# Kernel tuning notes

Hardware: AMD Instinct MI355X
Metric: run time of the kernel (lower is better)

Reference implementation:

```python
import jax, jax.numpy as jnp
import numpy as np

NB, HD, NL, NF = 5, 64, 4, 10           # num_bins, hidden_dim(d_model), num_layers, num_frames
DI, DS, DC, DTR = 128, 16, 4, 4          # d_inner=2*HD, d_state, d_conv, dt_rank=ceil(HD/16)
B, H, W = 4, 64, 64


def _conv2d(x, w, b):
    y = jax.lax.conv_general_dilated(x, w, (1, 1), 'SAME',
                                     dimension_numbers=('NCHW', 'OIHW', 'NCHW'))
    return y + b[None, :, None, None]


def _bn_relu(x, gamma, beta, eps=1e-5):
    # BatchNorm2d in training mode: biased batch stats over (N,H,W)
    mean = x.mean(axis=(0, 2, 3), keepdims=True)
    var = x.var(axis=(0, 2, 3), keepdims=True)
    y = (x - mean) * jax.lax.rsqrt(var + eps)
    return jax.nn.relu(y * gamma[None, :, None, None] + beta[None, :, None, None])


def _silu(x):
    return x * jax.nn.sigmoid(x)


def _causal_dwconv(x, w, b):
    # x: (B,L,DI), w: (DI,K) depthwise causal conv, b: (DI,)
    K = w.shape[1]
    L = x.shape[1]
    xp = jnp.pad(x, ((0, 0), (K - 1, 0), (0, 0)))
    y = sum(xp[:, k:k + L, :] * w[:, k] for k in range(K))
    return y + b


def _selective_scan(u, delta, A, Bm, Cm, D):
    # u,delta: (B,L,DI); A: (DI,DS); Bm,Cm: (B,L,DS); D: (DI,)
    dT, BT, CT, uT = (t.transpose(1, 0, 2) for t in (delta, Bm, Cm, u))
    h0 = jnp.zeros((u.shape[0], A.shape[0], A.shape[1]), u.dtype)

    def step(h, inp):
        d_t, B_t, C_t, u_t = inp                     # (B,DI),(B,DS),(B,DS),(B,DI)
        dA = jnp.exp(d_t[:, :, None] * A)            # (B,DI,DS)
        h = dA * h + (d_t * u_t)[:, :, None] * B_t[:, None, :]
        y = jnp.einsum('bds,bs->bd', h, C_t)
        return h, y

    _, ys = jax.lax.scan(step, h0, (dT, BT, CT, uT))  # ys: (L,B,DI)
    return ys.transpose(1, 0, 2) + u * D


def _mamba(x, in_proj, conv_w, conv_b, x_proj, dt_w, dt_b, A_log, Dp, out_proj):
    xz = x @ in_proj.T                               # (B,L,2*DI)
    xi, z = jnp.split(xz, 2, axis=-1)
    xi = _silu(_causal_dwconv(xi, conv_w, conv_b))
    xdbc = xi @ x_proj.T                             # (B,L,DTR+2*DS)
    dt, Bm, Cm = jnp.split(xdbc, [DTR, DTR + DS], axis=-1)
    delta = jax.nn.softplus(dt @ dt_w.T + dt_b)
    A = -jnp.exp(A_log)
    y = _selective_scan(xi, delta, A, Bm, Cm, Dp)
    return (y * _silu(z)) @ out_proj.T


def setup_inputs() -> dict:
    key = jax.random.key(0)
    ks = jax.random.split(key, 20)
    s = 0.02
    inp = {
        'x': jax.random.normal(ks[0], (B, NB, H, W), jnp.float32),
        'enc_w': jax.random.normal(ks[1], (HD, NB, 3, 3), jnp.float32) * s,
        'enc_b': jnp.zeros((HD,), jnp.float32),
        'enc_g': jnp.ones((HD,), jnp.float32),
        'enc_be': jnp.zeros((HD,), jnp.float32),
        'in_proj': jax.random.normal(ks[2], (NL, 2 * DI, HD), jnp.float32) * s,
        'conv_w': jax.random.normal(ks[3], (NL, DI, DC), jnp.float32) * s,
        'conv_b': jnp.zeros((NL, DI), jnp.float32),
        'x_proj': jax.random.normal(ks[4], (NL, DTR + 2 * DS, DI), jnp.float32) * s,
        'dt_w': jax.random.normal(ks[5], (NL, DI, DTR), jnp.float32) * s,
        'dt_b': jax.random.normal(ks[6], (NL, DI), jnp.float32) * 0.1 - 4.0,
        'A_log': jnp.broadcast_to(jnp.log(jnp.arange(1, DS + 1, dtype=jnp.float32)),
                                  (NL, DI, DS)).copy(),
        'Dp': jnp.ones((NL, DI), jnp.float32),
        'out_proj': jax.random.normal(ks[7], (NL, HD, DI), jnp.float32) * s,
        'dec1_w': jax.random.normal(ks[8], (HD, HD, 3, 3), jnp.float32) * s,
        'dec1_b': jnp.zeros((HD,), jnp.float32),
        'dec1_g': jnp.ones((HD,), jnp.float32),
        'dec1_be': jnp.zeros((HD,), jnp.float32),
        'dec2_w': jax.random.normal(ks[9], (NF, HD, 3, 3), jnp.float32) * s,
        'dec2_b': jnp.zeros((NF,), jnp.float32),
    }
    return inp


def reference(x, enc_w, enc_b, enc_g, enc_be, in_proj, conv_w, conv_b, x_proj,
              dt_w, dt_b, A_log, Dp, out_proj, dec1_w, dec1_b, dec1_g, dec1_be,
              dec2_w, dec2_b):
    Bb, _, Hh, Ww = x.shape
    h = _bn_relu(_conv2d(x, enc_w, enc_b), enc_g, enc_be)   # (B,HD,H,W)
    t = h.reshape(Bb, HD, Hh * Ww).transpose(0, 2, 1)        # (B,L,HD)
    for i in range(NL):
        t = t + _mamba(t, in_proj[i], conv_w[i], conv_b[i], x_proj[i],
                       dt_w[i], dt_b[i], A_log[i], Dp[i], out_proj[i])
    h = t.transpose(0, 2, 1).reshape(Bb, HD, Hh, Ww)
    h = _bn_relu(_conv2d(h, dec1_w, dec1_b), dec1_g, dec1_be)
    return _conv2d(h, dec2_w, dec2_b)                        # (B,NF,H,W)
```

## Files before the change

kernel.cpp:

```cpp
#include <hip/hip_runtime.h>
#include <hip/hip_bf16.h>

#define BB   4
#define NBC  5
#define HD   64
#define NLAYER 4
#define NFC  10
#define DIM  128
#define DSN  16
#define DCN  4
#define DTRK 4
#define HH   64
#define WWD  64
#define LL   4096
#define MM   (BB*LL)
#define NCHUNK 128
#define CLEN   32
#define TSTEP  16

__global__ void k_prep_all(const float* __restrict__ in_proj, const float* __restrict__ out_proj,
                           const float* __restrict__ dec1_w, const float* __restrict__ dec2_w,
                           float* __restrict__ wTin, float* __restrict__ wTout,
                           float* __restrict__ wT1, float* __restrict__ wT2,
                           float* __restrict__ stats, float* __restrict__ stats2) {
    int idx = blockIdx.x * blockDim.x + threadIdx.x;
    if (idx < 65536) {
        int n = idx & 255, k = (idx >> 8) & 63, l = idx >> 14;
        wTin[idx] = in_proj[(l << 14) + (n << 6) + k];
    } else if (idx < 98304) {
        int j = idx - 65536;
        int n = j & 63, k = (j >> 6) & 127, l = j >> 13;
        wTout[j] = out_proj[(l << 13) + (n << 7) + k];
    } else if (idx < 135168) {
        int j = idx - 98304;
        int co = j & 63, tap = (j >> 6) % 9, ci = j / 576;
        wT1[j] = dec1_w[co * 576 + ci * 9 + tap];
    } else if (idx < 142848) {
        int j = idx - 135168;
        int tap = j % 12, t2 = j / 12, co = t2 % NFC, ci = t2 / NFC;
        wT2[j] = (tap < 9) ? dec2_w[co * 576 + ci * 9 + tap] : 0.f;
    } else if (idx < 143104) {
        int j = idx - 142848;
        if (j < 128) stats[j] = 0.f; else stats2[j - 128] = 0.f;
    }
}

__global__ void k_enc_conv(const float* __restrict__ x, const float* __restrict__ w,
                           const float* __restrict__ bias, float* __restrict__ out,
                           float* __restrict__ stats) {
    __shared__ float r1[256], r2[256];
    int tid = threadIdx.x;
    int idx = blockIdx.x * 256 + tid;
    int wx = idx & 63;
    int hy = (idx >> 6) & 63;
    int co = (idx >> 12) & 63;
    int b  = idx >> 18;
    float acc = bias[co];
    for (int ci = 0; ci < NBC; ++ci) {
        const float* xin = x + (((long)(b * NBC + ci)) << 12);
        const float* wp  = w + (co * NBC + ci) * 9;
        #pragma unroll
        for (int kh = 0; kh < 3; ++kh) {
            int ih = hy + kh - 1;
            if (ih < 0 || ih >= HH) continue;
            #pragma unroll
            for (int kw = 0; kw < 3; ++kw) {
                int iw = wx + kw - 1;
                if (iw < 0 || iw >= WWD) continue;
                acc += xin[(ih << 6) + iw] * wp[kh * 3 + kw];
            }
        }
    }
    out[idx] = acc;
    r1[tid] = acc; r2[tid] = acc * acc;
    __syncthreads();
    for (int off = 128; off > 0; off >>= 1) {
        if (tid < off) { r1[tid] += r1[tid + off]; r2[tid] += r2[tid + off]; }
        __syncthreads();
    }
    if (tid == 0) {
        atomicAdd(&stats[co], r1[0]);
        atomicAdd(&stats[64 + co], r2[0]);
    }
}

__global__ __launch_bounds__(256, 1) void k_gemm_in_bn(const float* __restrict__ src,
                                                       const float* __restrict__ stats,
                                                       const float* __restrict__ g,
                                                       const float* __restrict__ be,
                                                       const float* __restrict__ wT,
                                                       float* __restrict__ tout,
                                                       float* __restrict__ xz) {
    __shared__ __align__(16) float ts[64 * 68];
    __shared__ float sc[64], sh[64];
    long m0 = (long)blockIdx.x << 6;
    int b = (int)(m0 >> 12);
    int hw0 = (int)(m0 & 4095);
    int tid = threadIdx.x;
    if (tid < 64) {
        float m = stats[tid] * (1.f / 16384.f);
        float var = stats[64 + tid] * (1.f / 16384.f) - m * m;
        float ss = g[tid] * rsqrtf(var + 1e-5f);
        sc[tid] = ss; sh[tid] = be[tid] - m * ss;
    }
    __syncthreads();
    for (int i = tid; i < 4096; i += 256) {
        int pix = i & 63, c = i >> 6;
        float v = src[(((long)((b << 6) + c)) << 12) + hw0 + pix];
        ts[pix * 68 + c] = fmaxf(v * sc[c] + sh[c], 0.f);
    }
    __syncthreads();
    for (int i = tid; i < 4096; i += 256) {
        int r = i >> 6, c = i & 63;
        tout[(m0 + r) * 64 + c] = ts[r * 68 + c];
    }
    int rg = tid >> 5;
    int cg = tid & 31;
    float acc[8][8] = {};
    int n0 = cg << 3;
    for (int k4 = 0; k4 < 16; ++k4) {
        float4 a[8];
        #pragma unroll
        for (int r2 = 0; r2 < 8; ++r2)
            a[r2] = *(const float4*)&ts[((rg << 3) + r2) * 68 + (k4 << 2)];
        #pragma unroll
        for (int kk = 0; kk < 4; ++kk) {
            const float* wr = wT + (((k4 << 2) + kk) << 8) + n0;
            float4 w0 = *(const float4*)&wr[0];
            float4 w1 = *(const float4*)&wr[4];
            #pragma unroll
            for (int r2 = 0; r2 < 8; ++r2) {
                float av = (kk == 0) ? a[r2].x : (kk == 1) ? a[r2].y
                         : (kk == 2) ? a[r2].z : a[r2].w;
                acc[r2][0] += av * w0.x; acc[r2][1] += av * w0.y;
                acc[r2][2] += av * w0.z; acc[r2][3] += av * w0.w;
                acc[r2][4] += av * w1.x; acc[r2][5] += av * w1.y;
                acc[r2][6] += av * w1.z; acc[r2][7] += av * w1.w;
            }
        }
    }
    #pragma unroll
    for (int r2 = 0; r2 < 8; ++r2) {
        long m = m0 + (rg << 3) + r2;
        *(float4*)&xz[(m << 8) + n0]     = make_float4(acc[r2][0], acc[r2][1], acc[r2][2], acc[r2][3]);
        *(float4*)&xz[(m << 8) + n0 + 4] = make_float4(acc[r2][4], acc[r2][5], acc[r2][6], acc[r2][7]);
    }
}

__global__ __launch_bounds__(256, 1) void k_gemm_oi(const float* __restrict__ gated,
                                                    const float* __restrict__ wTo,
                                                    const float* __restrict__ wTi,
                                                    float* __restrict__ tio,
                                                    float* __restrict__ xz) {
    __shared__ __align__(16) float g_s[64 * 132];
    __shared__ __align__(16) float t_s[64 * 68];
    long m0 = (long)blockIdx.x << 6;
    int tid = threadIdx.x;
    for (int i = tid; i < 8192; i += 256) {
        int r = i >> 7, k = i & 127;
        g_s[r * 132 + k] = gated[(m0 << 7) + i];
    }
    __syncthreads();
    {
        int rg = tid >> 4, cg = tid & 15;
        int n0 = cg << 2;
        float acc[4][4] = {};
        for (int k4 = 0; k4 < 32; ++k4) {
            float4 a[4];
            #pragma unroll
            for (int r2 = 0; r2 < 4; ++r2)
                a[r2] = *(const float4*)&g_s[((rg << 2) + r2) * 132 + (k4 << 2)];
            #pragma unroll
            for (int kk = 0; kk < 4; ++kk) {
                const float* wr = wTo + (((k4 << 2) + kk) << 6) + n0;
                float4 w0 = *(const float4*)&wr[0];
                #pragma unroll
                for (int r2 = 0; r2 < 4; ++r2) {
                    float av = (kk == 0) ? a[r2].x : (kk == 1) ? a[r2].y
                             : (kk == 2) ? a[r2].z : a[r2].w;
                    acc[r2][0] += av * w0.x; acc[r2][1] += av * w0.y;
                    acc[r2][2] += av * w0.z; acc[r2][3] += av * w0.w;
                }
            }
        }
        #pragma unroll
        for (int r2 = 0; r2 < 4; ++r2) {
            long m = m0 + (rg << 2) + r2;
            float4 t0 = *(const float4*)&tio[(m << 6) + n0];
            t0.x += acc[r2][0]; t0.y += acc[r2][1];
            t0.z += acc[r2][2]; t0.w += acc[r2][3];
            *(float4*)&tio[(m << 6) + n0] = t0;
            *(float4*)&t_s[((rg << 2) + r2) * 68 + n0] = t0;
        }
    }
    __syncthreads();
    {
        int rg = tid >> 5, cg = tid & 31;
        int n0 = cg << 3;
        float acc[8][8] = {};
        for (int k4 = 0; k4 < 16; ++k4) {
            float4 a[8];
            #pragma unroll
            for (int r2 = 0; r2 < 8; ++r2)
                a[r2] = *(const float4*)&t_s[((rg << 3) + r2) * 68 + (k4 << 2)];
            #pragma unroll
            for (int kk = 0; kk < 4; ++kk) {
                const float* wr = wTi + (((k4 << 2) + kk) << 8) + n0;
                float4 w0 = *(const float4*)&wr[0];
                float4 w1 = *(const float4*)&wr[4];
                #pragma unroll
                for (int r2 = 0; r2 < 8; ++r2) {
                    float av = (kk == 0) ? a[r2].x : (kk == 1) ? a[r2].y
                             : (kk == 2) ? a[r2].z : a[r2].w;
                    acc[r2][0] += av * w0.x; acc[r2][1] += av * w0.y;
                    acc[r2][2] += av * w0.z; acc[r2][3] += av * w0.w;
                    acc[r2][4] += av * w1.x; acc[r2][5] += av * w1.y;
                    acc[r2][6] += av * w1.z; acc[r2][7] += av * w1.w;
                }
            }
        }
        #pragma unroll
        for (int r2 = 0; r2 < 8; ++r2) {
            long m = m0 + (rg << 3) + r2;
            *(float4*)&xz[(m << 8) + n0]     = make_float4(acc[r2][0], acc[r2][1], acc[r2][2], acc[r2][3]);
            *(float4*)&xz[(m << 8) + n0 + 4] = make_float4(acc[r2][4], acc[r2][5], acc[r2][6], acc[r2][7]);
        }
    }
}

__global__ __launch_bounds__(256, 1) void k_gemm_out2(const float* __restrict__ gated,
                                                      const float* __restrict__ wT,
                                                      float* __restrict__ tio) {
    __shared__ __align__(16) float ts[64 * 132];
    long m0 = (long)blockIdx.x << 6;
    int tid = threadIdx.x;
    int rg = tid >> 4;
    int cg = tid & 15;
    for (int i = tid; i < 8192; i += 256) {
        int r2 = i >> 7, k = i & 127;
        ts[r2 * 132 + k] = gated[(m0 << 7) + i];
    }
    __syncthreads();
    float acc[4][4] = {};
    int n0 = cg << 2;
    for (int k4 = 0; k4 < 32; ++k4) {
        float4 a[4];
        #pragma unroll
        for (int r2 = 0; r2 < 4; ++r2)
            a[r2] = *(const float4*)&ts[((rg << 2) + r2) * 132 + (k4 << 2)];
        #pragma unroll
        for (int kk = 0; kk < 4; ++kk) {
            const float* wr = wT + (((k4 << 2) + kk) << 6) + n0;
            float4 w0 = *(const float4*)&wr[0];
            #pragma unroll
            for (int r2 = 0; r2 < 4; ++r2) {
                float av = (kk == 0) ? a[r2].x : (kk == 1) ? a[r2].y
                         : (kk == 2) ? a[r2].z : a[r2].w;
                acc[r2][0] += av * w0.x; acc[r2][1] += av * w0.y;
                acc[r2][2] += av * w0.z; acc[r2][3] += av * w0.w;
            }
        }
    }
    #pragma unroll
    for (int r2 = 0; r2 < 4; ++r2) {
        long m = m0 + (rg << 2) + r2;
        float4 t0 = *(const float4*)&tio[(m << 6) + n0];
        t0.x += acc[r2][0]; t0.y += acc[r2][1];
        t0.z += acc[r2][2]; t0.w += acc[r2][3];
        *(float4*)&tio[(m << 6) + n0] = t0;
    }
}

__global__ __launch_bounds__(256, 2) void k_xproj_fused(
        const float* __restrict__ xz, const float* __restrict__ cw,
        const float* __restrict__ cb, const float* __restrict__ Wx,
        const float* __restrict__ dw, const float* __restrict__ dbias,
        const float* __restrict__ A_log,
        float* __restrict__ xi, float* __restrict__ xdbc,
        float* __restrict__ delta, float* __restrict__ Pb, float* __restrict__ Sb) {
    __shared__ float xz_s[35 * 132];
    __shared__ float xi_s[32 * 132];
    __shared__ float w_s[36 * 132];
    __shared__ float xs[32 * 40];
    __shared__ float cwT[4 * 128];
    __shared__ float cb_s[128];
    long m0 = (long)blockIdx.x << 5;
    int l0 = (int)(m0 & 4095);
    int b = (int)(m0 >> 12);
    int chunk = l0 >> 5;
    int tid = threadIdx.x;

    for (int i = tid; i < 35 * 128; i += 256) {
        int j = i >> 7, k = i & 127;
        int l = l0 - 3 + j;
        float v = 0.f;
        if (l >= 0) v = xz[(m0 - 3 + j) * 256 + k];
        xz_s[j * 132 + k] = v;
    }
    if (tid < 128) cb_s[tid] = cb[tid];
    for (int i = tid; i < 512; i += 256) {
        int kk = i >> 7, di = i & 127;
        cwT[(kk << 7) + di] = cw[(di << 2) + kk];
    }
    for (int i = tid; i < 4608; i += 256) {
        int n = i >> 7, k = i & 127;
        w_s[n * 132 + k] = Wx[i];
    }
    __syncthreads();

    for (int ii = 0; ii < 4; ++ii) {
        int i = tid + (ii << 8);
        int r = i >> 5;
        int d4 = (i & 31) << 2;
        float4 a = *(const float4*)&cb_s[d4];
        #pragma unroll
        for (int kk = 0; kk < 4; ++kk) {
            float4 xv = *(const float4*)&xz_s[(r + kk) * 132 + d4];
            float4 wv = *(const float4*)&cwT[(kk << 7) + d4];
            a.x += xv.x * wv.x; a.y += xv.y * wv.y;
            a.z += xv.z * wv.z; a.w += xv.w * wv.w;
        }
        a.x = a.x / (1.f + __expf(-a.x));
        a.y = a.y / (1.f + __expf(-a.y));
        a.z = a.z / (1.f + __expf(-a.z));
        a.w = a.w / (1.f + __expf(-a.w));
        *(float4*)&xi_s[r * 132 + d4] = a;
        *(float4*)&xi[(m0 + r) * 128 + d4] = a;
    }
    __syncthreads();

    int n = tid & 63;
    int rg = tid >> 6;
    if (n < 36) {
        float acc[8] = {0,0,0,0,0,0,0,0};
        for (int k4 = 0; k4 < 32; ++k4) {
            float4 w4 = *(const float4*)&w_s[n * 132 + (k4 << 2)];
            #pragma unroll
            for (int r = 0; r < 8; ++r) {
                float4 a4 = *(const float4*)&xi_s[((rg << 3) + r) * 132 + (k4 << 2)];
                acc[r] += a4.x * w4.x + a4.y * w4.y + a4.z * w4.z + a4.w * w4.w;
            }
        }
        #pragma unroll
        for (int r = 0; r < 8; ++r) {
            int rr = (rg << 3) + r;
            xdbc[(m0 + rr) * 36 + n] = acc[r];
            xs[rr * 40 + n] = acc[r];
        }
    }
    __syncthreads();

    float* delta_s = xz_s;
    for (int i = tid; i < 4096; i += 256) {
        int r = i >> 7, di = i & 127;
        float v = dbias[di];
        float4 d4 = *(const float4*)&dw[di << 2];
        v += xs[r * 40 + 0] * d4.x + xs[r * 40 + 1] * d4.y
           + xs[r * 40 + 2] * d4.z + xs[r * 40 + 3] * d4.w;
        float sp = (v > 20.f) ? v : log1pf(expf(v));
        delta[(m0 + r) * 128 + di] = sp;
        delta_s[r * 132 + di] = sp;
    }
    __syncthreads();

    {
        int di = tid >> 1;
        int dso = (tid & 1) << 3;
        float4 al0 = *(const float4*)&A_log[(di << 4) + dso];
        float4 al1 = *(const float4*)&A_log[(di << 4) + dso + 4];
        float Av[8] = { -expf(al0.x), -expf(al0.y), -expf(al0.z), -expf(al0.w),
                        -expf(al1.x), -expf(al1.y), -expf(al1.z), -expf(al1.w) };
        float h[8] = {0,0,0,0,0,0,0,0};
        float P[8] = {1,1,1,1,1,1,1,1};
        #pragma unroll 4
        for (int i = 0; i < CLEN; ++i) {
            float d = delta_s[i * 132 + di];
            float u = xi_s[i * 132 + di];
            float du = d * u;
            float4 B0 = *(float4*)&xs[i * 40 + DTRK + dso];
            float4 B1 = *(float4*)&xs[i * 40 + DTRK + dso + 4];
            float a0 = __expf(d * Av[0]); h[0] = a0 * h[0] + du * B0.x; P[0] *= a0;
            float a1 = __expf(d * Av[1]); h[1] = a1 * h[1] + du * B0.y; P[1] *= a1;
            float a2 = __expf(d * Av[2]); h[2] = a2 * h[2] + du * B0.z; P[2] *= a2;
            float a3 = __expf(d * Av[3]); h[3] = a3 * h[3] + du * B0.w; P[3] *= a3;
            float a4 = __expf(d * Av[4]); h[4] = a4 * h[4] + du * B1.x; P[4] *= a4;
            float a5 = __expf(d * Av[5]); h[5] = a5 * h[5] + du * B1.y; P[5] *= a5;
            float a6 = __expf(d * Av[6]); h[6] = a6 * h[6] + du * B1.z; P[6] *= a6;
            float a7 = __expf(d * Av[7]); h[7] = a7 * h[7] + du * B1.w; P[7] *= a7;
        }
        long o = (((long)chunk * BB + b) << 11) + (di << 4) + dso;
        *(float4*)&Pb[o]     = make_float4(P[0], P[1], P[2], P[3]);
        *(float4*)&Pb[o + 4] = make_float4(P[4], P[5], P[6], P[7]);
        *(float4*)&Sb[o]     = make_float4(h[0], h[1], h[2], h[3]);
        *(float4*)&Sb[o + 4] = make_float4(h[4], h[5], h[6], h[7]);
    }
}

__global__ void k_scan_p2(float* Pb, const float* __restrict__ Sb) {
    int t = blockIdx.x * blockDim.x + threadIdx.x;
    int b = t >> 11;
    int s = t & 2047;
    float h = 0.f;
    for (int c = 0; c < NCHUNK; ++c) {
        long idx = (((long)c * BB + b) << 11) + s;
        float p = Pb[idx];
        float sv = Sb[idx];
        Pb[idx] = h;
        h = p * h + sv;
    }
}

__global__ void k_scan_p3(const float* __restrict__ delta, const float* __restrict__ xi,
                          const float* __restrict__ xdbc, const float* __restrict__ A_log,
                          const float* __restrict__ Dp, const float* __restrict__ xz,
                          const float* __restrict__ hin, float* __restrict__ gated) {
    __shared__ float d_s[TSTEP][64];
    __shared__ float u_s[TSTEP][64];
    __shared__ float bc_s[TSTEP][32];
    __shared__ float y_s[TSTEP][64];
    int chunk = blockIdx.x, b = blockIdx.y, half = blockIdx.z;
    int tid = threadIdx.x;
    int dq = tid & 3;
    int dil = tid >> 2;
    int di = (half << 6) + dil;
    float4 al = *(const float4*)&A_log[(di << 4) + (dq << 2)];
    float Av[4] = { -expf(al.x), -expf(al.y), -expf(al.z), -expf(al.w) };
    float Dv = Dp[di];
    long ho = (((long)chunk * BB + b) << 11) + (di << 4) + (dq << 2);
    float4 h4 = *(const float4*)&hin[ho];
    float h[4] = { h4.x, h4.y, h4.z, h4.w };
    long t0 = ((long)b << 12) + (long)chunk * CLEN;

    int srow = tid >> 4, sc4 = (tid & 15) << 2;
    for (int tile = 0; tile < CLEN / TSTEP; ++tile) {
        __syncthreads();
        long ls = t0 + tile * TSTEP + srow;
        *(float4*)&d_s[srow][sc4] = *(const float4*)&delta[(ls << 7) + (half << 6) + sc4];
        *(float4*)&u_s[srow][sc4] = *(const float4*)&xi[(ls << 7) + (half << 6) + sc4];
        if (tid < 128) {
            int r2 = tid >> 3, cc = (tid & 7) << 2;
            long l2 = t0 + tile * TSTEP + r2;
            *(float4*)&bc_s[r2][cc] = *(const float4*)&xdbc[l2 * 36 + DTRK + cc];
        }
        __syncthreads();
        #pragma unroll
        for (int i = 0; i < TSTEP; ++i) {
            float d = d_s[i][dil];
            float u = u_s[i][dil];
            float du = d * u;
            float4 Bv = *(float4*)&bc_s[i][dq << 2];
            float4 Cv = *(float4*)&bc_s[i][16 + (dq << 2)];
            float a0 = __expf(d * Av[0]); h[0] = a0 * h[0] + du * Bv.x;
            float a1 = __expf(d * Av[1]); h[1] = a1 * h[1] + du * Bv.y;
            float a2 = __expf(d * Av[2]); h[2] = a2 * h[2] + du * Bv.z;
            float a3 = __expf(d * Av[3]); h[3] = a3 * h[3] + du * Bv.w;
            float yp = h[0] * Cv.x + h[1] * Cv.y + h[2] * Cv.z + h[3] * Cv.w;
            yp += __shfl_xor(yp, 1);
            yp += __shfl_xor(yp, 2);
            if (dq == 0)
                y_s[i][dil] = yp + u * Dv;
        }
        __syncthreads();
        {
            long l = t0 + tile * TSTEP + srow;
            float4 y4 = *(float4*)&y_s[srow][sc4];
            float4 z4 = *(const float4*)&xz[(l << 8) + DIM + (half << 6) + sc4];
            float4 og;
            og.x = y4.x * (z4.x / (1.f + __expf(-z4.x)));
            og.y = y4.y * (z4.y / (1.f + __expf(-z4.y)));
            og.z = y4.z * (z4.z / (1.f + __expf(-z4.z)));
            og.w = y4.w * (z4.w / (1.f + __expf(-z4.w)));
            *(float4*)&gated[(l << 7) + (half << 6) + sc4] = og;
        }
    }
}

__global__ __launch_bounds__(256, 1) void k_dec1_new(const float* __restrict__ tin,
                                                     const float* __restrict__ wT,
                                                     const float* __restrict__ bias,
                                                     float* __restrict__ out,
                                                     float* __restrict__ stats2) {
    __shared__ __align__(16) float x_s[64 * 132];
    __shared__ __align__(16) float w_s[4 * 4608];
    int tile = blockIdx.x;
    int b = blockIdx.y;
    int ty0 = (tile >> 3) << 3;
    int tx0 = (tile & 7) << 3;
    int tid = threadIdx.x;
    int wv = tid >> 6;
    int lane = tid & 63;
    int r = lane >> 3;
    int cg = lane & 7;

    for (int i = tid; i < 6400; i += 256) {
        int pl = i >> 6;
        int c = i & 63;
        int py = pl / 10, px = pl - py * 10;
        int ih = ty0 + py - 1, iw = tx0 + px - 1;
        float v = 0.f;
        if (ih >= 0 && ih < HH && iw >= 0 && iw < WWD)
            v = tin[(((long)((b << 12) + (ih << 6) + iw)) << 6) + c];
        x_s[c * 132 + py * 12 + px] = v;
    }
    float* myw = &w_s[wv * 4608];
    const float* gw = wT + (wv * 16) * 576;
    float4 pref[18];
    #pragma unroll
    for (int i = 0; i < 18; ++i)
        pref[i] = *(const float4*)&gw[(i * 64 + lane) * 4];
    #pragma unroll
    for (int i = 0; i < 18; ++i)
        *(float4*)&myw[(i * 64 + lane) * 4] = pref[i];
    __syncthreads();

    float acc[8][8] = {};
    #pragma unroll
    for (int ch = 0; ch < 2; ++ch) {
        if (ch == 0) {
            const float* gw1 = wT + (wv * 16 + 8) * 576;
            #pragma unroll
            for (int i = 0; i < 18; ++i)
                pref[i] = *(const float4*)&gw1[(i * 64 + lane) * 4];
        }
        for (int cl = 0; cl < 8; ++cl) {
            int cib = wv * 16 + ch * 8 + cl;
            float xrow[3][10];
            #pragma unroll
            for (int kh = 0; kh < 3; ++kh) {
                const float* xr = &x_s[cib * 132 + (r + kh) * 12];
                float4 a0 = *(const float4*)&xr[0];
                float4 a1 = *(const float4*)&xr[4];
                float2 a2 = *(const float2*)&xr[8];
                xrow[kh][0] = a0.x; xrow[kh][1] = a0.y; xrow[kh][2] = a0.z; xrow[kh][3] = a0.w;
                xrow[kh][4] = a1.x; xrow[kh][5] = a1.y; xrow[kh][6] = a1.z; xrow[kh][7] = a1.w;
                xrow[kh][8] = a2.x; xrow[kh][9] = a2.y;
            }
            const float* wp = &myw[cl * 576];
            #pragma unroll
            for (int kh = 0; kh < 3; ++kh) {
                #pragma unroll
                for (int kw = 0; kw < 3; ++kw) {
                    const float* wp2 = wp + (kh * 3 + kw) * 64 + (cg << 3);
                    float4 wa = *(const float4*)&wp2[0];
                    float4 wb = *(const float4*)&wp2[4];
                    #pragma unroll
                    for (int j = 0; j < 8; ++j) {
                        float xv = xrow[kh][kw + j];
                        acc[j][0] += xv * wa.x; acc[j][1] += xv * wa.y;
                        acc[j][2] += xv * wa.z; acc[j][3] += xv * wa.w;
                        acc[j][4] += xv * wb.x; acc[j][5] += xv * wb.y;
                        acc[j][6] += xv * wb.z; acc[j][7] += xv * wb.w;
                    }
                }
            }
        }
        if (ch == 0) {
            #pragma unroll
            for (int i = 0; i < 18; ++i)
                *(float4*)&myw[(i * 64 + lane) * 4] = pref[i];
        }
    }

    #pragma unroll
    for (int j = 0; j < 8; ++j) {
        *(float4*)&myw[lane * 68 + (j << 3)]     = make_float4(acc[j][0], acc[j][1], acc[j][2], acc[j][3]);
        *(float4*)&myw[lane * 68 + (j << 3) + 4] = make_float4(acc[j][4], acc[j][5], acc[j][6], acc[j][7]);
    }
    __syncthreads();

    float bv = bias[lane];
    float ssum = 0.f, ssq = 0.f;
    #pragma unroll
    for (int pp = 0; pp < 16; ++pp) {
        int pr = (wv << 1) + (pp >> 3);
        int pc = pp & 7;
        int ol = (pr << 3) + (lane >> 3);
        int ix = (pc << 3) + (lane & 7);
        float s = w_s[ol * 68 + ix] + w_s[4608 + ol * 68 + ix]
                + w_s[9216 + ol * 68 + ix] + w_s[13824 + ol * 68 + ix] + bv;
        out[(((long)((b << 12) + ((ty0 + pr) << 6) + tx0 + pc)) << 6) + lane] = s;
        ssum += s; ssq += s * s;
    }
    float* red = x_s;
    red[(wv << 6) + lane] = ssum;
    red[256 + (wv << 6) + lane] = ssq;
    __syncthreads();
    if (tid < 64) {
        float a = red[tid] + red[64 + tid] + red[128 + tid] + red[192 + tid];
        float q = red[256 + tid] + red[320 + tid] + red[384 + tid] + red[448 + tid];
        atomicAdd(&stats2[tid], a);
        atomicAdd(&stats2[64 + tid], q);
    }
}

__global__ void k_dec2_fused(const float* __restrict__ src, const float* __restrict__ stats2,
                             const float* __restrict__ g, const float* __restrict__ be,
                             const float* __restrict__ wT, const float* __restrict__ bias,
                             float* __restrict__ out) {
    __shared__ float x_s[64 * 101];
    __shared__ float w_s[64 * NFC * 12];
    __shared__ float sc_s[64];
    __shared__ float sh_s[64];
    int tile = blockIdx.x;
    int b = blockIdx.y;
    int ty0 = (tile >> 3) << 3;
    int tx0 = (tile & 7) << 3;
    int tid = threadIdx.x;

    if (tid < 64) {
        float m = stats2[tid] * (1.f / 16384.f);
        float var = stats2[64 + tid] * (1.f / 16384.f) - m * m;
        float s = g[tid] * rsqrtf(var + 1e-5f);
        sc_s[tid] = s;
        sh_s[tid] = be[tid] - m * s;
    }
    for (int i = tid; i < 64 * NFC * 12; i += 256)
        w_s[i] = wT[i];
    __syncthreads();

    for (int i = tid; i < 6400; i += 256) {
        int pl = i >> 6;
        int c = i & 63;
        int py = pl / 10, px = pl - py * 10;
        int ih = ty0 + py - 1, iw = tx0 + px - 1;
        float v = 0.f;
        if (ih >= 0 && ih < HH && iw >= 0 && iw < WWD) {
            v = src[((long)((b << 12) + (ih << 6) + iw)) * 64 + c];
            v = fmaxf(v * sc_s[c] + sh_s[c], 0.f);
        }
        x_s[c * 101 + pl] = v;
    }
    __syncthreads();

    int px = tid & 63;
    int py = px >> 3, pxx = px & 7;
    int cog = tid >> 6;
    float acc[3] = {0.f, 0.f, 0.f};
    int nco = (cog < 2) ? 3 : 2;

    for (int ci = 0; ci < 64; ++ci) {
        const float* xr = &x_s[ci * 101 + py * 10 + pxx];
        float xv[9];
        #pragma unroll
        for (int kh = 0; kh < 3; ++kh)
            #pragma unroll
            for (int kw = 0; kw < 3; ++kw)
                xv[kh * 3 + kw] = xr[kh * 10 + kw];
        #pragma unroll
        for (int j = 0; j < 3; ++j) {
            if (j >= nco) break;
            int co = cog + (j << 2);
            const float* wp = &w_s[(ci * NFC + co) * 12];
            float4 w0 = *(const float4*)&wp[0];
            float4 w1 = *(const float4*)&wp[4];
            float  w8 = wp[8];
            acc[j] += xv[0] * w0.x + xv[1] * w0.y + xv[2] * w0.z + xv[3] * w0.w
                    + xv[4] * w1.x + xv[5] * w1.y + xv[6] * w1.z + xv[7] * w1.w
                    + xv[8] * w8;
        }
    }
    int hw = ((ty0 + py) << 6) + tx0 + pxx;
    #pragma unroll
    for (int j = 0; j < 3; ++j) {
        if (j >= nco) break;
        int co = cog + (j << 2);
        out[((long)(b * NFC + co) << 12) + hw] = acc[j] + bias[co];
    }
}

extern "C" void kernel_launch(void* const* d_in, const int* in_sizes, int n_in,
                              void* d_out, int out_size, void* d_ws, size_t ws_size,
                              hipStream_t stream) {
    const float* x       = (const float*)d_in[0];
    const float* enc_w   = (const float*)d_in[1];
    const float* enc_b   = (const float*)d_in[2];
    const float* enc_g   = (const float*)d_in[3];
    const float* enc_be  = (const float*)d_in[4];
    const float* in_proj = (const float*)d_in[5];
    const float* conv_w  = (const float*)d_in[6];
    const float* conv_b  = (const float*)d_in[7];
    const float* x_proj  = (const float*)d_in[8];
    const float* dt_w    = (const float*)d_in[9];
    const float* dt_b    = (const float*)d_in[10];
    const float* A_log   = (const float*)d_in[11];
    const float* Dp      = (const float*)d_in[12];
    const float* out_prj = (const float*)d_in[13];
    const float* dec1_w  = (const float*)d_in[14];
    const float* dec1_b  = (const float*)d_in[15];
    const float* dec1_g  = (const float*)d_in[16];
    const float* dec1_be = (const float*)d_in[17];
    const float* dec2_w  = (const float*)d_in[18];
    const float* dec2_b  = (const float*)d_in[19];
    float* out = (float*)d_out;

    float* ws = (float*)d_ws;
    size_t off = 0;
    float* conv_buf  = ws + off; off += 1048576;
    float* stats     = ws + off; off += 128;
    float* stats2    = ws + off; off += 128;
    float* wT1       = ws + off; off += 36864;
    float* wT2       = ws + off; off += 7680;
    float* wTin      = ws + off; off += 65536;
    float* wTout     = ws + off; off += 32768;
    float* t_buf     = ws + off; off += 1048576;
    float* xz_buf    = ws + off; off += 4194304;
    float* xi_buf    = ws + off; off += 2097152;
    float* xdbc_buf  = ws + off; off += 589824;
    float* delta_buf = ws + off; off += 2097152;
    float* gated_buf = ws + off; off += 2097152;
    (void)ws_size; (void)in_sizes; (void)n_in; (void)out_size;

    float* Pb = conv_buf;
    float* Sb = gated_buf;

    k_prep_all<<<560, 256, 0, stream>>>(in_proj, out_prj, dec1_w, dec2_w,
                                        wTin, wTout, wT1, wT2, stats, stats2);

    k_enc_conv<<<4096, 256, 0, stream>>>(x, enc_w, enc_b, conv_buf, stats);

    dim3 sg(NCHUNK, BB, 2);
    k_gemm_in_bn<<<256, 256, 0, stream>>>(conv_buf, stats, enc_g, enc_be, wTin, t_buf, xz_buf);
    for (int i = 0; i < NLAYER; ++i) {
        k_xproj_fused<<<512, 256, 0, stream>>>(xz_buf, conv_w + i * DIM * DCN,
                                               conv_b + i * DIM, x_proj + i * 36 * DIM,
                                               dt_w + i * DIM * DTRK, dt_b + i * DIM,
                                               A_log + i * DIM * DSN,
                                               xi_buf, xdbc_buf, delta_buf, Pb, Sb);
        k_scan_p2<<<32, 256, 0, stream>>>(Pb, Sb);
        k_scan_p3<<<sg, 256, 0, stream>>>(delta_buf, xi_buf, xdbc_buf,
                                          A_log + i * DIM * DSN, Dp + i * DIM,
                                          xz_buf, Pb, gated_buf);
        if (i < NLAYER - 1)
            k_gemm_oi<<<256, 256, 0, stream>>>(gated_buf, wTout + i * 8192,
                                               wTin + (i + 1) * 16384, t_buf, xz_buf);
    }
    k_gemm_out2<<<256, 256, 0, stream>>>(gated_buf, wTout + 3 * 8192, t_buf);

    dim3 dg1(64, BB);
    k_dec1_new<<<dg1, 256, 0, stream>>>(t_buf, wT1, dec1_b, conv_buf, stats2);
    k_dec2_fused<<<dg1, 256, 0, stream>>>(conv_buf, stats2, dec1_g, dec1_be, wT2, dec2_b, out);
}
```

Before: 509.2 us.

## Fuse scan phase 3 with out-proj and next-layer in-proj GEMMs

The per-chunk scan output kernel now keeps the full 128-channel chunk in shared memory. In the same block it applies the SiLU(z) gate, the out_proj GEMM with residual add, and, except on the last layer, the next layer's in_proj GEMM. This removes the gated buffer round trip through global memory and the separate GEMM launches per layer. The trade-offs: each thread now scans 8 states instead of 4, blocks cover 32 rows instead of 64 so weight reuse per block is lower, and shared-memory use per block grows.

```diff
diff --git a/kernel.cpp b/kernel.cpp
--- a/kernel.cpp
+++ b/kernel.cpp
@@ -147,130 +147,6 @@
     }
 }
 
-__global__ __launch_bounds__(256, 1) void k_gemm_oi(const float* __restrict__ gated,
-                                                    const float* __restrict__ wTo,
-                                                    const float* __restrict__ wTi,
-                                                    float* __restrict__ tio,
-                                                    float* __restrict__ xz) {
-    __shared__ __align__(16) float g_s[64 * 132];
-    __shared__ __align__(16) float t_s[64 * 68];
-    long m0 = (long)blockIdx.x << 6;
-    int tid = threadIdx.x;
-    for (int i = tid; i < 8192; i += 256) {
-        int r = i >> 7, k = i & 127;
-        g_s[r * 132 + k] = gated[(m0 << 7) + i];
-    }
-    __syncthreads();
-    {
-        int rg = tid >> 4, cg = tid & 15;
-        int n0 = cg << 2;
-        float acc[4][4] = {};
-        for (int k4 = 0; k4 < 32; ++k4) {
-            float4 a[4];
-            #pragma unroll
-            for (int r2 = 0; r2 < 4; ++r2)
-                a[r2] = *(const float4*)&g_s[((rg << 2) + r2) * 132 + (k4 << 2)];
-            #pragma unroll
-            for (int kk = 0; kk < 4; ++kk) {
-                const float* wr = wTo + (((k4 << 2) + kk) << 6) + n0;
-                float4 w0 = *(const float4*)&wr[0];
-                #pragma unroll
-                for (int r2 = 0; r2 < 4; ++r2) {
-                    float av = (kk == 0) ? a[r2].x : (kk == 1) ? a[r2].y
-                             : (kk == 2) ? a[r2].z : a[r2].w;
-                    acc[r2][0] += av * w0.x; acc[r2][1] += av * w0.y;
-                    acc[r2][2] += av * w0.z; acc[r2][3] += av * w0.w;
-                }
-            }
-        }
-        #pragma unroll
-        for (int r2 = 0; r2 < 4; ++r2) {
-            long m = m0 + (rg << 2) + r2;
-            float4 t0 = *(const float4*)&tio[(m << 6) + n0];
-            t0.x += acc[r2][0]; t0.y += acc[r2][1];
-            t0.z += acc[r2][2]; t0.w += acc[r2][3];
-            *(float4*)&tio[(m << 6) + n0] = t0;
-            *(float4*)&t_s[((rg << 2) + r2) * 68 + n0] = t0;
-        }
-    }
-    __syncthreads();
-    {
-        int rg = tid >> 5, cg = tid & 31;
-        int n0 = cg << 3;
-        float acc[8][8] = {};
-        for (int k4 = 0; k4 < 16; ++k4) {
-            float4 a[8];
-            #pragma unroll
-            for (int r2 = 0; r2 < 8; ++r2)
-                a[r2] = *(const float4*)&t_s[((rg << 3) + r2) * 68 + (k4 << 2)];
-            #pragma unroll
-            for (int kk = 0; kk < 4; ++kk) {
-                const float* wr = wTi + (((k4 << 2) + kk) << 8) + n0;
-                float4 w0 = *(const float4*)&wr[0];
-                float4 w1 = *(const float4*)&wr[4];
-                #pragma unroll
-                for (int r2 = 0; r2 < 8; ++r2) {
-                    float av = (kk == 0) ? a[r2].x : (kk == 1) ? a[r2].y
-                             : (kk == 2) ? a[r2].z : a[r2].w;
-                    acc[r2][0] += av * w0.x; acc[r2][1] += av * w0.y;
-                    acc[r2][2] += av * w0.z; acc[r2][3] += av * w0.w;
-                    acc[r2][4] += av * w1.x; acc[r2][5] += av * w1.y;
-                    acc[r2][6] += av * w1.z; acc[r2][7] += av * w1.w;
-                }
-            }
-        }
-        #pragma unroll
-        for (int r2 = 0; r2 < 8; ++r2) {
-            long m = m0 + (rg << 3) + r2;
-            *(float4*)&xz[(m << 8) + n0]     = make_float4(acc[r2][0], acc[r2][1], acc[r2][2], acc[r2][3]);
-            *(float4*)&xz[(m << 8) + n0 + 4] = make_float4(acc[r2][4], acc[r2][5], acc[r2][6], acc[r2][7]);
-        }
-    }
-}
-
-__global__ __launch_bounds__(256, 1) void k_gemm_out2(const float* __restrict__ gated,
-                                                      const float* __restrict__ wT,
-                                                      float* __restrict__ tio) {
-    __shared__ __align__(16) float ts[64 * 132];
-    long m0 = (long)blockIdx.x << 6;
-    int tid = threadIdx.x;
-    int rg = tid >> 4;
-    int cg = tid & 15;
-    for (int i = tid; i < 8192; i += 256) {
-        int r2 = i >> 7, k = i & 127;
-        ts[r2 * 132 + k] = gated[(m0 << 7) + i];
-    }
-    __syncthreads();
-    float acc[4][4] = {};
-    int n0 = cg << 2;
-    for (int k4 = 0; k4 < 32; ++k4) {
-        float4 a[4];
-        #pragma unroll
-        for (int r2 = 0; r2 < 4; ++r2)
-            a[r2] = *(const float4*)&ts[((rg << 2) + r2) * 132 + (k4 << 2)];
-        #pragma unroll
-        for (int kk = 0; kk < 4; ++kk) {
-            const float* wr = wT + (((k4 << 2) + kk) << 6) + n0;
-            float4 w0 = *(const float4*)&wr[0];
-            #pragma unroll
-            for (int r2 = 0; r2 < 4; ++r2) {
-                float av = (kk == 0) ? a[r2].x : (kk == 1) ? a[r2].y
-                         : (kk == 2) ? a[r2].z : a[r2].w;
-                acc[r2][0] += av * w0.x; acc[r2][1] += av * w0.y;
-                acc[r2][2] += av * w0.z; acc[r2][3] += av * w0.w;
-            }
-        }
-    }
-    #pragma unroll
-    for (int r2 = 0; r2 < 4; ++r2) {
-        long m = m0 + (rg << 2) + r2;
-        float4 t0 = *(const float4*)&tio[(m << 6) + n0];
-        t0.x += acc[r2][0]; t0.y += acc[r2][1];
-        t0.z += acc[r2][2]; t0.w += acc[r2][3];
-        *(float4*)&tio[(m << 6) + n0] = t0;
-    }
-}
-
 __global__ __launch_bounds__(256, 2) void k_xproj_fused(
         const float* __restrict__ xz, const float* __restrict__ cw,
         const float* __restrict__ cb, const float* __restrict__ Wx,
@@ -410,67 +286,144 @@
     }
 }
 
-__global__ void k_scan_p3(const float* __restrict__ delta, const float* __restrict__ xi,
-                          const float* __restrict__ xdbc, const float* __restrict__ A_log,
-                          const float* __restrict__ Dp, const float* __restrict__ xz,
-                          const float* __restrict__ hin, float* __restrict__ gated) {
-    __shared__ float d_s[TSTEP][64];
-    __shared__ float u_s[TSTEP][64];
-    __shared__ float bc_s[TSTEP][32];
-    __shared__ float y_s[TSTEP][64];
-    int chunk = blockIdx.x, b = blockIdx.y, half = blockIdx.z;
+__global__ __launch_bounds__(256, 1) void k_scan_p3_oi(
+        const float* __restrict__ delta, const float* __restrict__ xi,
+        const float* __restrict__ xdbc, const float* __restrict__ A_log,
+        const float* __restrict__ Dp, const float* __restrict__ xz,
+        const float* __restrict__ hin, const float* __restrict__ wTo,
+        const float* __restrict__ wTi, float* __restrict__ tio,
+        float* __restrict__ xz_out, int doB) {
+    __shared__ __align__(16) float d_s[32 * 132];
+    __shared__ __align__(16) float u_s[32 * 132];
+    __shared__ __align__(16) float bc_s[32 * 36];
+    __shared__ __align__(16) float t_s[32 * 68];
+    int chunk = blockIdx.x, b = blockIdx.y;
     int tid = threadIdx.x;
-    int dq = tid & 3;
-    int dil = tid >> 2;
-    int di = (half << 6) + dil;
-    float4 al = *(const float4*)&A_log[(di << 4) + (dq << 2)];
-    float Av[4] = { -expf(al.x), -expf(al.y), -expf(al.z), -expf(al.w) };
+    long t0 = ((long)b << 12) + (long)chunk * CLEN;
+
+    for (int i = tid; i < 1024; i += 256) {
+        int r = i >> 5, c4 = (i & 31) << 2;
+        *(float4*)&d_s[r * 132 + c4] = *(const float4*)&delta[(t0 + r) * 128 + c4];
+        *(float4*)&u_s[r * 132 + c4] = *(const float4*)&xi[(t0 + r) * 128 + c4];
+    }
+    {
+        int r = tid >> 3, c4 = (tid & 7) << 2;
+        *(float4*)&bc_s[r * 36 + c4] = *(const float4*)&xdbc[(t0 + r) * 36 + DTRK + c4];
+    }
+
+    int di = tid >> 1;
+    int dso = (tid & 1) << 3;
+    float4 al0 = *(const float4*)&A_log[(di << 4) + dso];
+    float4 al1 = *(const float4*)&A_log[(di << 4) + dso + 4];
+    float Av[8] = { -expf(al0.x), -expf(al0.y), -expf(al0.z), -expf(al0.w),
+                    -expf(al1.x), -expf(al1.y), -expf(al1.z), -expf(al1.w) };
     float Dv = Dp[di];
-    long ho = (((long)chunk * BB + b) << 11) + (di << 4) + (dq << 2);
-    float4 h4 = *(const float4*)&hin[ho];
-    float h[4] = { h4.x, h4.y, h4.z, h4.w };
-    long t0 = ((long)b << 12) + (long)chunk * CLEN;
-
-    int srow = tid >> 4, sc4 = (tid & 15) << 2;
-    for (int tile = 0; tile < CLEN / TSTEP; ++tile) {
-        __syncthreads();
-        long ls = t0 + tile * TSTEP + srow;
-        *(float4*)&d_s[srow][sc4] = *(const float4*)&delta[(ls << 7) + (half << 6) + sc4];
-        *(float4*)&u_s[srow][sc4] = *(const float4*)&xi[(ls << 7) + (half << 6) + sc4];
-        if (tid < 128) {
-            int r2 = tid >> 3, cc = (tid & 7) << 2;
-            long l2 = t0 + tile * TSTEP + r2;
-            *(float4*)&bc_s[r2][cc] = *(const float4*)&xdbc[l2 * 36 + DTRK + cc];
-        }
-        __syncthreads();
-        #pragma unroll
-        for (int i = 0; i < TSTEP; ++i) {
-            float d = d_s[i][dil];
-            float u = u_s[i][dil];
-            float du = d * u;
-            float4 Bv = *(float4*)&bc_s[i][dq << 2];
-            float4 Cv = *(float4*)&bc_s[i][16 + (dq << 2)];
-            float a0 = __expf(d * Av[0]); h[0] = a0 * h[0] + du * Bv.x;
-            float a1 = __expf(d * Av[1]); h[1] = a1 * h[1] + du * Bv.y;
-            float a2 = __expf(d * Av[2]); h[2] = a2 * h[2] + du * Bv.z;
-            float a3 = __expf(d * Av[3]); h[3] = a3 * h[3] + du * Bv.w;
-            float yp = h[0] * Cv.x + h[1] * Cv.y + h[2] * Cv.z + h[3] * Cv.w;
-            yp += __shfl_xor(yp, 1);
-            yp += __shfl_xor(yp, 2);
-            if (dq == 0)
-                y_s[i][dil] = yp + u * Dv;
-        }
-        __syncthreads();
-        {
-            long l = t0 + tile * TSTEP + srow;
-            float4 y4 = *(float4*)&y_s[srow][sc4];
-            float4 z4 = *(const float4*)&xz[(l << 8) + DIM + (half << 6) + sc4];
-            float4 og;
-            og.x = y4.x * (z4.x / (1.f + __expf(-z4.x)));
-            og.y = y4.y * (z4.y / (1.f + __expf(-z4.y)));
-            og.z = y4.z * (z4.z / (1.f + __expf(-z4.z)));
-            og.w = y4.w * (z4.w / (1.f + __expf(-z4.w)));
-            *(float4*)&gated[(l << 7) + (half << 6) + sc4] = og;
+    long o = (((long)chunk * BB + b) << 11) + (di << 4) + dso;
+    float4 h0 = *(const float4*)&hin[o];
+    float4 h1 = *(const float4*)&hin[o + 4];
+    float h[8] = { h0.x, h0.y, h0.z, h0.w, h1.x, h1.y, h1.z, h1.w };
+    __syncthreads();
+
+    #pragma unroll 4
+    for (int i = 0; i < CLEN; ++i) {
+        float d = d_s[i * 132 + di];
+        float u = u_s[i * 132 + di];
+        float du = d * u;
+        const float* bc = &bc_s[i * 36];
+        float4 B0 = *(const float4*)&bc[dso];
+        float4 B1 = *(const float4*)&bc[dso + 4];
+        float4 C0 = *(const float4*)&bc[16 + dso];
+        float4 C1 = *(const float4*)&bc[16 + dso + 4];
+        float a0 = __expf(d * Av[0]); h[0] = a0 * h[0] + du * B0.x;
+        float a1 = __expf(d * Av[1]); h[1] = a1 * h[1] + du * B0.y;
+        float a2 = __expf(d * Av[2]); h[2] = a2 * h[2] + du * B0.z;
+        float a3 = __expf(d * Av[3]); h[3] = a3 * h[3] + du * B0.w;
+        float a4 = __expf(d * Av[4]); h[4] = a4 * h[4] + du * B1.x;
+        float a5 = __expf(d * Av[5]); h[5] = a5 * h[5] + du * B1.y;
+        float a6 = __expf(d * Av[6]); h[6] = a6 * h[6] + du * B1.z;
+        float a7 = __expf(d * Av[7]); h[7] = a7 * h[7] + du * B1.w;
+        float yp = h[0] * C0.x + h[1] * C0.y + h[2] * C0.z + h[3] * C0.w
+                 + h[4] * C1.x + h[5] * C1.y + h[6] * C1.z + h[7] * C1.w;
+        yp += __shfl_xor(yp, 1);
+        if (dso == 0)
+            u_s[i * 132 + di] = yp + u * Dv;
+    }
+    __syncthreads();
+
+    for (int i = tid; i < 1024; i += 256) {
+        int r = i >> 5, c4 = (i & 31) << 2;
+        float4 y4 = *(float4*)&u_s[r * 132 + c4];
+        float4 z4 = *(const float4*)&xz[((t0 + r) << 8) + DIM + c4];
+        y4.x *= z4.x / (1.f + __expf(-z4.x));
+        y4.y *= z4.y / (1.f + __expf(-z4.y));
+        y4.z *= z4.z / (1.f + __expf(-z4.z));
+        y4.w *= z4.w / (1.f + __expf(-z4.w));
+        *(float4*)&u_s[r * 132 + c4] = y4;
+    }
+    __syncthreads();
+
+    {
+        int rg = tid >> 4, cg = tid & 15;
+        int n0 = cg << 2;
+        float acc[2][4] = {};
+        for (int k4 = 0; k4 < 32; ++k4) {
+            float4 a0 = *(const float4*)&u_s[(rg << 1) * 132 + (k4 << 2)];
+            float4 a1 = *(const float4*)&u_s[((rg << 1) + 1) * 132 + (k4 << 2)];
+            #pragma unroll
+            for (int kk = 0; kk < 4; ++kk) {
+                const float* wr = wTo + (((k4 << 2) + kk) << 6) + n0;
+                float4 w0 = *(const float4*)&wr[0];
+                float av0 = (kk == 0) ? a0.x : (kk == 1) ? a0.y : (kk == 2) ? a0.z : a0.w;
+                float av1 = (kk == 0) ? a1.x : (kk == 1) ? a1.y : (kk == 2) ? a1.z : a1.w;
+                acc[0][0] += av0 * w0.x; acc[0][1] += av0 * w0.y;
+                acc[0][2] += av0 * w0.z; acc[0][3] += av0 * w0.w;
+                acc[1][0] += av1 * w0.x; acc[1][1] += av1 * w0.y;
+                acc[1][2] += av1 * w0.z; acc[1][3] += av1 * w0.w;
+            }
+        }
+        #pragma unroll
+        for (int r2 = 0; r2 < 2; ++r2) {
+            long m = t0 + (rg << 1) + r2;
+            float4 tv = *(const float4*)&tio[(m << 6) + n0];
+            tv.x += acc[r2][0]; tv.y += acc[r2][1];
+            tv.z += acc[r2][2]; tv.w += acc[r2][3];
+            *(float4*)&tio[(m << 6) + n0] = tv;
+            *(float4*)&t_s[((rg << 1) + r2) * 68 + n0] = tv;
+        }
+    }
+    if (!doB) return;
+    __syncthreads();
+
+    {
+        int rg = tid >> 5, cgn = tid & 31;
+        int n0 = cgn << 3;
+        float acc[4][8] = {};
+        for (int k4 = 0; k4 < 16; ++k4) {
+            float4 a[4];
+            #pragma unroll
+            for (int r2 = 0; r2 < 4; ++r2)
+                a[r2] = *(const float4*)&t_s[((rg << 2) + r2) * 68 + (k4 << 2)];
+            #pragma unroll
+            for (int kk = 0; kk < 4; ++kk) {
+                const float* wr = wTi + (((k4 << 2) + kk) << 8) + n0;
+                float4 w0 = *(const float4*)&wr[0];
+                float4 w1 = *(const float4*)&wr[4];
+                #pragma unroll
+                for (int r2 = 0; r2 < 4; ++r2) {
+                    float av = (kk == 0) ? a[r2].x : (kk == 1) ? a[r2].y
+                             : (kk == 2) ? a[r2].z : a[r2].w;
+                    acc[r2][0] += av * w0.x; acc[r2][1] += av * w0.y;
+                    acc[r2][2] += av * w0.z; acc[r2][3] += av * w0.w;
+                    acc[r2][4] += av * w1.x; acc[r2][5] += av * w1.y;
+                    acc[r2][6] += av * w1.z; acc[r2][7] += av * w1.w;
+                }
+            }
+        }
+        #pragma unroll
+        for (int r2 = 0; r2 < 4; ++r2) {
+            long m = t0 + (rg << 2) + r2;
+            *(float4*)&xz_out[(m << 8) + n0]     = make_float4(acc[r2][0], acc[r2][1], acc[r2][2], acc[r2][3]);
+            *(float4*)&xz_out[(m << 8) + n0 + 4] = make_float4(acc[r2][4], acc[r2][5], acc[r2][6], acc[r2][7]);
         }
     }
 }
@@ -707,19 +660,19 @@
     float* xi_buf    = ws + off; off += 2097152;
     float* xdbc_buf  = ws + off; off += 589824;
     float* delta_buf = ws + off; off += 2097152;
-    float* gated_buf = ws + off; off += 2097152;
+    float* Sb_buf    = ws + off; off += 1048576;
     (void)ws_size; (void)in_sizes; (void)n_in; (void)out_size;
 
     float* Pb = conv_buf;
-    float* Sb = gated_buf;
+    float* Sb = Sb_buf;
 
     k_prep_all<<<560, 256, 0, stream>>>(in_proj, out_prj, dec1_w, dec2_w,
                                         wTin, wTout, wT1, wT2, stats, stats2);
 
     k_enc_conv<<<4096, 256, 0, stream>>>(x, enc_w, enc_b, conv_buf, stats);
 
-    dim3 sg(NCHUNK, BB, 2);
     k_gemm_in_bn<<<256, 256, 0, stream>>>(conv_buf, stats, enc_g, enc_be, wTin, t_buf, xz_buf);
+    dim3 pg(NCHUNK, BB);
     for (int i = 0; i < NLAYER; ++i) {
         k_xproj_fused<<<512, 256, 0, stream>>>(xz_buf, conv_w + i * DIM * DCN,
                                                conv_b + i * DIM, x_proj + i * 36 * DIM,
@@ -727,14 +680,13 @@
                                                A_log + i * DIM * DSN,
                                                xi_buf, xdbc_buf, delta_buf, Pb, Sb);
         k_scan_p2<<<32, 256, 0, stream>>>(Pb, Sb);
-        k_scan_p3<<<sg, 256, 0, stream>>>(delta_buf, xi_buf, xdbc_buf,
-                                          A_log + i * DIM * DSN, Dp + i * DIM,
-                                          xz_buf, Pb, gated_buf);
-        if (i < NLAYER - 1)
-            k_gemm_oi<<<256, 256, 0, stream>>>(gated_buf, wTout + i * 8192,
-                                               wTin + (i + 1) * 16384, t_buf, xz_buf);
-    }
-    k_gemm_out2<<<256, 256, 0, stream>>>(gated_buf, wTout + 3 * 8192, t_buf);
+        int doB = (i < NLAYER - 1) ? 1 : 0;
+        k_scan_p3_oi<<<pg, 256, 0, stream>>>(delta_buf, xi_buf, xdbc_buf,
+                                             A_log + i * DIM * DSN, Dp + i * DIM,
+                                             xz_buf, Pb, wTout + i * 8192,
+                                             wTin + ((i + 1) & 3) * 16384,
+                                             t_buf, xz_buf, doB);
+    }
 
     dim3 dg1(64, BB);
     k_dec1_new<<<dg1, 256, 0, stream>>>(t_buf, wT1, dec1_b, conv_buf, stats2);
```

New measurement: 489.8 us. 3.8% less time.
